# Kernel tuning notes

Measured on AMD Instinct MI355X. Metric: run time of the kernel, lower is better.

The kernel has to match this reference:

```python
import jax, jax.numpy as jnp
import numpy as np


def _rbf_kernel(X, Z, variance, lengthscale):
    # K[n, r] = variance * exp(-||x_n - z_r||^2 / (2 * lengthscale^2))
    x2 = jnp.sum(X * X, axis=-1)[:, None]          # [N, 1]
    z2 = jnp.sum(Z * Z, axis=-1)[None, :]          # [1, R]
    sq = x2 + z2 - 2.0 * (X @ Z.T)                 # [N, R]
    sq = jnp.maximum(sq, 0.0)
    return variance * jnp.exp(-0.5 * sq / (lengthscale * lengthscale))


def setup_inputs() -> dict:
    key = jax.random.key(0)
    ks = jax.random.split(key, 6)
    N, D, S, F, R = 16384, 8, 8, 1024, 2048
    X_star = jax.random.normal(ks[0], (N, D), dtype=jnp.float32)
    ref_points = jax.random.normal(ks[1], (R, D), dtype=jnp.float32)
    omega = jax.random.normal(ks[2], (S, D, F), dtype=jnp.float32)
    two_pi = 2.0 * np.pi
    phase = jax.random.uniform(ks[3], (S, F), dtype=jnp.float32) * two_pi
    feature_weights = jax.random.normal(ks[4], (S, F), dtype=jnp.float32)
    correction_weights = jax.random.normal(ks[5], (S, R), dtype=jnp.float32)
    variance = jnp.ones((), dtype=jnp.float32)
    lengthscale = jnp.ones((), dtype=jnp.float32)
    return {
        "X_star": X_star,
        "ref_points": ref_points,
        "omega": omega,
        "phase": phase,
        "feature_weights": feature_weights,
        "correction_weights": correction_weights,
        "variance": variance,
        "lengthscale": lengthscale,
    }


def reference(X_star, ref_points, omega, phase, feature_weights,
              correction_weights, variance, lengthscale):
    F = omega.shape[-1]
    # RFF prior paths: angles [S, N, F]
    angles = jnp.einsum('nd,sdf->snf', X_star, omega) / lengthscale + phase[:, None, :]
    scale = jnp.sqrt(2.0 * variance / F)
    features = scale * jnp.cos(angles)                       # [S, N, F]
    prior = jnp.sum(features * feature_weights[:, None, :], axis=-1)  # [S, N]
    # Kernel correction term
    K_cross = _rbf_kernel(X_star, ref_points, variance, lengthscale)  # [N, R]
    update = jnp.einsum('nr,sr->sn', K_cross, correction_weights)     # [S, N]
    # mean_fn is None -> zero mean
    mean = jnp.zeros(X_star.shape[0], dtype=X_star.dtype)
    return prior + update + mean[None, :]
```

## Files before the change

### kernel.cpp

```cpp
#include <hip/hip_runtime.h>
#include <math.h>

#ifndef __has_builtin
#define __has_builtin(x) 0
#endif

typedef __attribute__((ext_vector_type(8))) short bf16x8;
typedef __attribute__((ext_vector_type(4))) float f32x4;

__device__ __forceinline__ float fast_fract(float x) {
#if __has_builtin(__builtin_amdgcn_fractf)
    return __builtin_amdgcn_fractf(x);
#else
    return x - floorf(x);
#endif
}
__device__ __forceinline__ float fast_cos2pi(float x) {
#if __has_builtin(__builtin_amdgcn_cosf)
    return __builtin_amdgcn_cosf(x);
#else
    return cosf(x * 6.28318530717958647692f);
#endif
}
__device__ __forceinline__ float fast_exp2(float x) {
#if __has_builtin(__builtin_amdgcn_exp2f)
    return __builtin_amdgcn_exp2f(x);
#else
    return exp2f(x);
#endif
}
__device__ __forceinline__ unsigned short f2bf(float f) {
    unsigned u = __float_as_uint(f);
    return (unsigned short)((u + 0x7FFFu + ((u >> 16) & 1u)) >> 16);
}
__device__ __forceinline__ float bf2f(unsigned short b) {
    return __uint_as_float(((unsigned)b) << 16);
}
__device__ __forceinline__ unsigned packbf(float lo, float hi) {
    return (unsigned)f2bf(lo) | ((unsigned)f2bf(hi) << 16);
}

constexpr int kN = 16384, kD = 8, kS = 8, kF = 1024, kR = 2048;
constexpr float kInv2Pi = 0.15915494309189535f;
constexpr float kLog2e  = 1.4426950408889634f;
constexpr int kWsPrior = 512, kWsZ = 128, kWsCw = 64;
constexpr int kWsTiles = kWsPrior + kWsZ + kWsCw;
constexpr size_t kWsNeed = (size_t)kWsTiles * 64 * 16;

__global__ __launch_bounds__(256)
void prep_kernel(const float* __restrict__ omega, const float* __restrict__ phase,
                 const float* __restrict__ Z, const float* __restrict__ cw,
                 const float* __restrict__ lsp, uint4* __restrict__ ws)
{
    const int job  = blockIdx.x * 256 + threadIdx.x;
    const int lane = job & 63;
    const int tile = job >> 6;
    const int g = lane >> 4, c = lane & 15;

    const float inv_ls = 1.0f / lsp[0];
    const float m_ang  = kInv2Pi * inv_ls;
    const float L      = kLog2e * inv_ls * inv_ls;

    unsigned short h[8];
    if (tile < kWsPrior) {
        const int s = tile >> 6, ft = tile & 63, f = ft * 16 + c;
        const float* om = omega + s * (kD * kF);
        const float* ph = phase + s * kF;
        #pragma unroll
        for (int j = 0; j < 8; ++j) {
            const int k = g * 8 + j;
            unsigned short v = 0;
            if (k < 16) {
                v = f2bf(om[(k & 7) * kF + f] * m_ang);
            } else if (k < 24) {
                const float w = om[(k - 16) * kF + f] * m_ang;
                v = f2bf(w - bf2f(f2bf(w)));
            } else if (k == 24) {
                v = f2bf(ph[f] * kInv2Pi);
            } else if (k == 25) {
                const float p = ph[f] * kInv2Pi;
                v = f2bf(p - bf2f(f2bf(p)));
            }
            h[j] = v;
        }
    } else if (tile < kWsPrior + kWsZ) {
        const int rt = tile - kWsPrior;
        const int r  = rt * 16 + c;
        const float* zr = Z + r * kD;
        float zz = 0.f;
        #pragma unroll
        for (int d = 0; d < kD; ++d) zz = fmaf(zr[d], zr[d], zz);
        const float ztv = -0.5f * L * zz;
        #pragma unroll
        for (int j = 0; j < 8; ++j) {
            const int k = g * 8 + j;
            unsigned short v = 0;
            if (k < 8) {
                v = f2bf(L * zr[k]);
            } else if (k < 16) {
                v = f2bf(L * zr[k - 8]);
            } else if (k < 24) {
                const float w = L * zr[k - 16];
                v = f2bf(w - bf2f(f2bf(w)));
            } else if (k == 24) {
                v = f2bf(ztv);
            } else if (k == 25) {
                v = f2bf(ztv - bf2f(f2bf(ztv)));
            } else if (k < 28) {
                v = 0x3F80;
            }
            h[j] = v;
        }
    } else {
        const int rb = tile - kWsPrior - kWsZ;
        const int r0 = rb * 32;
        #pragma unroll
        for (int j = 0; j < 8; ++j)
            h[j] = (c < 8) ? f2bf(cw[c * kR + r0 + g * 8 + j]) : (unsigned short)0;
    }
    uint4 w;
    w.x = (unsigned)h[0] | ((unsigned)h[1] << 16);
    w.y = (unsigned)h[2] | ((unsigned)h[3] << 16);
    w.z = (unsigned)h[4] | ((unsigned)h[5] << 16);
    w.w = (unsigned)h[6] | ((unsigned)h[7] << 16);
    ws[tile * 64 + lane] = w;
}

__device__ __forceinline__ bf16x8 build_af_x(const float* __restrict__ X,
                                             int row, int g)
{
    float xv[kD];
    const float4 x0 = *reinterpret_cast<const float4*>(X + row * kD);
    const float4 x1 = *reinterpret_cast<const float4*>(X + row * kD + 4);
    xv[0]=x0.x; xv[1]=x0.y; xv[2]=x0.z; xv[3]=x0.w;
    xv[4]=x1.x; xv[5]=x1.y; xv[6]=x1.z; xv[7]=x1.w;
    bf16x8 af;
    if (g == 1) {
        #pragma unroll
        for (int j = 0; j < 8; ++j)
            af[j] = (short)f2bf(xv[j] - bf2f(f2bf(xv[j])));
    } else {
        #pragma unroll
        for (int j = 0; j < 8; ++j) af[j] = (short)f2bf(xv[j]);
    }
    return af;
}

__global__ __launch_bounds__(512, 4)
void prior_mfma3(const float* __restrict__ X, const float* __restrict__ fw,
                 const float* __restrict__ varp, const uint4* __restrict__ wsP,
                 float* __restrict__ out)
{
    __shared__ uint4 lds_b[4096];
    __shared__ float lds_fw[kF];
    const int tid  = threadIdx.x;
    const int lane = tid & 63;
    const int wave = __builtin_amdgcn_readfirstlane(tid >> 6);
    const int s  = blockIdx.y;
    const int c = lane & 15, g = lane >> 4;
    const int n0 = blockIdx.x * 256 + wave * 32;

    {
        const uint4* src = wsP + s * 4096;
        #pragma unroll
        for (int it = 0; it < 8; ++it)
            lds_b[it * 512 + tid] = src[it * 512 + tid];
        const float* fws = fw + s * kF;
        lds_fw[tid]       = fws[tid];
        lds_fw[tid + 512] = fws[tid + 512];
    }

    bf16x8 af0, af1;
    if (g == 3) {
        #pragma unroll
        for (int j = 0; j < 8; ++j) { af0[j] = 0; af1[j] = 0; }
        af0[0] = (short)0x3F80; af0[1] = (short)0x3F80;
        af1[0] = (short)0x3F80; af1[1] = (short)0x3F80;
    } else {
        af0 = build_af_x(X, n0 + c, g);
        af1 = build_af_x(X, n0 + 16 + c, g);
    }

    const float scale = sqrtf(2.0f * varp[0] / (float)kF);

    __syncthreads();

    float acc[2][4];
    #pragma unroll
    for (int t = 0; t < 2; ++t)
        #pragma unroll
        for (int r = 0; r < 4; ++r) acc[t][r] = 0.f;

    const uint4* lb = lds_b + lane;
    #pragma unroll 2
    for (int ft = 0; ft < 64; ++ft) {
        const bf16x8 bw = __builtin_bit_cast(bf16x8, lb[ft * 64]);
        const float fwv = lds_fw[ft * 16 + c];
        const f32x4 d0 = __builtin_amdgcn_mfma_f32_16x16x32_bf16(
            af0, bw, (f32x4){0.f, 0.f, 0.f, 0.f}, 0, 0, 0);
        const f32x4 d1 = __builtin_amdgcn_mfma_f32_16x16x32_bf16(
            af1, bw, (f32x4){0.f, 0.f, 0.f, 0.f}, 0, 0, 0);
        #pragma unroll
        for (int r = 0; r < 4; ++r) {
            acc[0][r] = fmaf(fwv, fast_cos2pi(fast_fract(d0[r])), acc[0][r]);
            acc[1][r] = fmaf(fwv, fast_cos2pi(fast_fract(d1[r])), acc[1][r]);
        }
    }

    #pragma unroll
    for (int m = 1; m <= 8; m <<= 1)
        #pragma unroll
        for (int t = 0; t < 2; ++t)
            #pragma unroll
            for (int r = 0; r < 4; ++r)
                acc[t][r] += __shfl_xor(acc[t][r], m);

    if (c == 0) {
        #pragma unroll
        for (int t = 0; t < 2; ++t) {
            float* o = out + s * kN + n0 + t * 16 + g * 4;
            #pragma unroll
            for (int r = 0; r < 4; ++r) o[r] = scale * acc[t][r];
        }
    }
}

__global__ __launch_bounds__(256, 2)
void update_mfma3(const float* __restrict__ X, const float* __restrict__ varp,
                  const float* __restrict__ lsp, const uint4* __restrict__ wsZ,
                  const uint4* __restrict__ wsC, float* __restrict__ out)
{
    __shared__ unsigned b2raw[4][256];
    __shared__ f32x4 red[2][2][2][16];
    const int tid  = threadIdx.x;
    const int lane = tid & 63;
    const int w    = __builtin_amdgcn_readfirstlane(tid >> 6);
    const int tl   = w >> 1, half = w & 1;
    const int tile = blockIdx.x * 2 + tl;
    const int n0   = tile * 16;
    const int c = lane & 15, g = lane >> 4;

    const float inv_ls = 1.0f / lsp[0];
    const float L = kLog2e * inv_ls * inv_ls;

    bf16x8 bf1;
    {
        float xv[kD];
        const float4 x0 = *reinterpret_cast<const float4*>(X + (n0 + c) * kD);
        const float4 x1 = *reinterpret_cast<const float4*>(X + (n0 + c) * kD + 4);
        xv[0]=x0.x; xv[1]=x0.y; xv[2]=x0.z; xv[3]=x0.w;
        xv[4]=x1.x; xv[5]=x1.y; xv[6]=x1.z; xv[7]=x1.w;
        if (g == 3) {
            float xx = 0.f;
            #pragma unroll
            for (int d = 0; d < kD; ++d) xx = fmaf(xv[d], xv[d], xx);
            const float xt = -0.5f * L * xx;
            const unsigned short th = f2bf(xt);
            const unsigned short tlw = f2bf(xt - bf2f(th));
            #pragma unroll
            for (int j = 0; j < 8; ++j) bf1[j] = 0;
            bf1[0] = (short)0x3F80; bf1[1] = (short)0x3F80;
            bf1[2] = (short)th;     bf1[3] = (short)tlw;
        } else if (g == 1) {
            #pragma unroll
            for (int j = 0; j < 8; ++j)
                bf1[j] = (short)f2bf(xv[j] - bf2f(f2bf(xv[j])));
        } else {
            #pragma unroll
            for (int j = 0; j < 8; ++j) bf1[j] = (short)f2bf(xv[j]);
        }
    }

    const int wbase = (g >> 1) * 64 + c * 4 + (g & 1) * 2;
    const int rbase = (g >> 1) * 128 + (g & 1) * 64 + c * 4;
    unsigned* bb = &b2raw[w][0];

    const uint4* zp = wsZ + lane;
    const uint4* cp = wsC + lane;
    const int rb0 = half * 32;

    f32x4 acc = {0.f, 0.f, 0.f, 0.f};
    uint4 za = zp[(rb0 * 2) * 64];
    uint4 zb = zp[(rb0 * 2 + 1) * 64];
    uint4 cf = cp[rb0 * 64];

    for (int i = 0; i < 32; ++i) {
        const int rb = rb0 + i;
        const int rbn = (i < 31) ? rb + 1 : rb;
        const uint4 zan = zp[(rbn * 2) * 64];
        const uint4 zbn = zp[(rbn * 2 + 1) * 64];
        const uint4 cfn = cp[rbn * 64];

        const f32x4 e0 = __builtin_amdgcn_mfma_f32_16x16x32_bf16(
            __builtin_bit_cast(bf16x8, za), bf1, (f32x4){0.f,0.f,0.f,0.f}, 0, 0, 0);
        const f32x4 e1 = __builtin_amdgcn_mfma_f32_16x16x32_bf16(
            __builtin_bit_cast(bf16x8, zb), bf1, (f32x4){0.f,0.f,0.f,0.f}, 0, 0, 0);

        float K0[4], K1[4];
        #pragma unroll
        for (int r = 0; r < 4; ++r) {
            K0[r] = fast_exp2(fminf(e0[r], 0.f));
            K1[r] = fast_exp2(fminf(e1[r], 0.f));
        }
        const unsigned p0 = packbf(K0[0], K0[1]);
        const unsigned p1 = packbf(K0[2], K0[3]);
        const unsigned p2 = packbf(K1[0], K1[1]);
        const unsigned p3 = packbf(K1[2], K1[3]);

        uint2 w0; w0.x = p0; w0.y = p1;
        uint2 w1; w1.x = p2; w1.y = p3;
        *reinterpret_cast<uint2*>(&bb[wbase])       = w0;
        *reinterpret_cast<uint2*>(&bb[wbase + 128]) = w1;
        const uint4 b2w = *reinterpret_cast<const uint4*>(&bb[rbase]);

        acc = __builtin_amdgcn_mfma_f32_16x16x32_bf16(
            __builtin_bit_cast(bf16x8, cf), __builtin_bit_cast(bf16x8, b2w),
            acc, 0, 0, 0);

        za = zan; zb = zbn; cf = cfn;
    }

    if (g < 2) red[tl][half][g][c] = acc;
    __syncthreads();

    {
        const int tl2 = tid >> 7, s = (tid >> 4) & 7, n = tid & 15;
        const float sum = red[tl2][0][s >> 2][n][s & 3]
                        + red[tl2][1][s >> 2][n][s & 3];
        const int idx = s * kN + (blockIdx.x * 2 + tl2) * 16 + n;
        out[idx] = fmaf(varp[0], sum, out[idx]);
    }
}

__global__ __launch_bounds__(512, 8)
void prior_fb(const float* __restrict__ X, const float* __restrict__ omega,
              const float* __restrict__ phase, const float* __restrict__ fw,
              const float* __restrict__ varp, const float* __restrict__ lsp,
              float* __restrict__ out)
{
    const int tid  = threadIdx.x;
    const int nloc = tid & 63;
    const int wave = __builtin_amdgcn_readfirstlane(tid >> 6);
    const int s    = blockIdx.y;
    const int n    = blockIdx.x * 64 + nloc;
    const float variance = varp[0];
    const float inv_ls   = 1.0f / lsp[0];
    const float scale = sqrtf(2.0f * variance / (float)kF);
    float xa[kD];
    {
        const float4 x0 = *reinterpret_cast<const float4*>(X + n * kD);
        const float4 x1 = *reinterpret_cast<const float4*>(X + n * kD + 4);
        const float m = inv_ls * kInv2Pi;
        xa[0]=x0.x*m; xa[1]=x0.y*m; xa[2]=x0.z*m; xa[3]=x0.w*m;
        xa[4]=x1.x*m; xa[5]=x1.y*m; xa[6]=x1.z*m; xa[7]=x1.w*m;
    }
    const float* om  = omega + s * (kD * kF);
    const float* ph  = phase + s * kF;
    const float* fwp = fw    + s * kF;
    const int f0 = wave * 128;
    float acc0 = 0.f, acc1 = 0.f;
    for (int fb = f0; fb < f0 + 128; fb += 8) {
        float cv[8];
        #pragma unroll
        for (int j = 0; j < 8; ++j) {
            float t = ph[fb + j] * kInv2Pi;
            #pragma unroll
            for (int d = 0; d < kD; ++d) t = fmaf(xa[d], om[d * kF + fb + j], t);
            cv[j] = fast_cos2pi(fast_fract(t));
        }
        #pragma unroll
        for (int j = 0; j < 8; j += 2) {
            acc0 = fmaf(fwp[fb + j], cv[j], acc0);
            acc1 = fmaf(fwp[fb + j + 1], cv[j + 1], acc1);
        }
    }
    __shared__ float red[8][64];
    red[wave][nloc] = acc0 + acc1;
    __syncthreads();
    if (tid < 64) {
        float t = 0.f;
        #pragma unroll
        for (int k = 0; k < 8; ++k) t += red[k][tid];
        out[s * kN + blockIdx.x * 64 + tid] = scale * t;
    }
}

__global__ __launch_bounds__(1024, 8)
void update_fb(const float* __restrict__ X, const float* __restrict__ Z,
               const float* __restrict__ cw, const float* __restrict__ varp,
               const float* __restrict__ lsp, float* __restrict__ out)
{
    const int tid  = threadIdx.x;
    const int nloc = tid & 63;
    const int wave = __builtin_amdgcn_readfirstlane(tid >> 6);
    const int n    = blockIdx.x * 64 + nloc;
    const float variance = varp[0];
    const float inv_ls   = 1.0f / lsp[0];
    const float L = kLog2e * inv_ls * inv_ls;
    __shared__ float zt_lds[kR];
    __shared__ float red[16][64][kS + 1];
    float x[kD];
    {
        const float4 x0 = *reinterpret_cast<const float4*>(X + n * kD);
        const float4 x1 = *reinterpret_cast<const float4*>(X + n * kD + 4);
        x[0]=x0.x; x[1]=x0.y; x[2]=x0.z; x[3]=x0.w;
        x[4]=x1.x; x[5]=x1.y; x[6]=x1.z; x[7]=x1.w;
    }
    for (int r = tid; r < kR; r += 1024) {
        const float4 z0 = *reinterpret_cast<const float4*>(Z + r * kD);
        const float4 z1 = *reinterpret_cast<const float4*>(Z + r * kD + 4);
        float z2 = z0.x*z0.x + z0.y*z0.y + z0.z*z0.z + z0.w*z0.w
                 + z1.x*z1.x + z1.y*z1.y + z1.z*z1.z + z1.w*z1.w;
        zt_lds[r] = -0.5f * L * z2;
    }
    __syncthreads();
    float xb[kD]; float x2 = 0.f;
    #pragma unroll
    for (int d = 0; d < kD; ++d) { xb[d] = x[d] * L; x2 = fmaf(x[d], x[d], x2); }
    const float xt = -0.5f * L * x2;
    float accU[2][kS];
    #pragma unroll
    for (int j = 0; j < kS; ++j) { accU[0][j] = 0.f; accU[1][j] = 0.f; }
    const int r0 = wave * 128;
    #pragma unroll 4
    for (int rr = 0; rr < 128; ++rr) {
        const int r = r0 + rr;
        float e = xt + zt_lds[r];
        #pragma unroll
        for (int d = 0; d < kD; ++d) e = fmaf(xb[d], Z[r * kD + d], e);
        e = fminf(e, 0.f);
        const float K = fast_exp2(e);
        #pragma unroll
        for (int j = 0; j < kS; ++j)
            accU[rr & 1][j] = fmaf(K, cw[j * kR + r], accU[rr & 1][j]);
    }
    #pragma unroll
    for (int j = 0; j < kS; ++j) red[wave][nloc][j] = accU[0][j] + accU[1][j];
    __syncthreads();
    if (tid < 512) {
        const int n2 = tid & 63;
        const int jj = tid >> 6;
        float tot = 0.f;
        #pragma unroll
        for (int k = 0; k < 16; ++k) tot += red[k][n2][jj];
        const int idx = jj * kN + blockIdx.x * 64 + n2;
        out[idx] = fmaf(variance, tot, out[idx]);
    }
}

extern "C" void kernel_launch(void* const* d_in, const int* in_sizes, int n_in,
                              void* d_out, int out_size, void* d_ws, size_t ws_size,
                              hipStream_t stream) {
    const float* X  = (const float*)d_in[0];
    const float* Z  = (const float*)d_in[1];
    const float* om = (const float*)d_in[2];
    const float* ph = (const float*)d_in[3];
    const float* fw = (const float*)d_in[4];
    const float* cw = (const float*)d_in[5];
    const float* vp = (const float*)d_in[6];
    const float* lp = (const float*)d_in[7];
    float* out = (float*)d_out;

    if (ws_size >= kWsNeed) {
        uint4* wsP = (uint4*)d_ws;
        uint4* wsZ = wsP + (size_t)kWsPrior * 64;
        uint4* wsC = wsP + (size_t)(kWsPrior + kWsZ) * 64;
        hipLaunchKernelGGL(prep_kernel, dim3(176), dim3(256), 0, stream,
                           om, ph, Z, cw, lp, wsP);
        hipLaunchKernelGGL(prior_mfma3, dim3(64, 8), dim3(512), 0, stream,
                           X, fw, vp, wsP, out);
        hipLaunchKernelGGL(update_mfma3, dim3(512), dim3(256), 0, stream,
                           X, vp, lp, wsZ, wsC, out);
    } else {
        hipLaunchKernelGGL(prior_fb, dim3(kN / 64, kS), dim3(512), 0, stream,
                           X, om, ph, fw, vp, lp, out);
        hipLaunchKernelGGL(update_fb, dim3(kN / 64), dim3(1024), 0, stream,
                           X, Z, cw, vp, lp, out);
    }
}
```

Before: 107.3 us.

## Fuse prior and update kernels into one interleaved launch with atomic accumulation

Merges the RFF prior kernel and the kernel-correction update kernel into a single launch whose blocks alternate between prior work (two of every three) and update work. The output is zeroed by extra blocks in the prep kernel, and both paths accumulate with atomicAdd, so the two phases no longer serialize across a kernel boundary and one launch is removed. The prior path now streams weights straight from global memory with a one-step register prefetch instead of staging them in LDS, which raises occupancy but adds global and atomic traffic.

```diff
diff --git a/kernel.cpp b/kernel.cpp
--- a/kernel.cpp
+++ b/kernel.cpp
@@ -50,8 +50,17 @@
 __global__ __launch_bounds__(256)
 void prep_kernel(const float* __restrict__ omega, const float* __restrict__ phase,
                  const float* __restrict__ Z, const float* __restrict__ cw,
-                 const float* __restrict__ lsp, uint4* __restrict__ ws)
+                 const float* __restrict__ lsp, uint4* __restrict__ ws,
+                 float* __restrict__ out)
 {
+    if (blockIdx.x >= 176) {
+        const int zid = (blockIdx.x - 176) * 256 + threadIdx.x;
+        float4* o4 = reinterpret_cast<float4*>(out);
+        #pragma unroll
+        for (int j = 0; j < 4; ++j)
+            o4[zid * 4 + j] = (float4){0.f, 0.f, 0.f, 0.f};
+        return;
+    }
     const int job  = blockIdx.x * 256 + threadIdx.x;
     const int lane = job & 63;
     const int tile = job >> 6;
@@ -146,189 +155,173 @@
     return af;
 }
 
-__global__ __launch_bounds__(512, 4)
-void prior_mfma3(const float* __restrict__ X, const float* __restrict__ fw,
-                 const float* __restrict__ varp, const uint4* __restrict__ wsP,
-                 float* __restrict__ out)
-{
-    __shared__ uint4 lds_b[4096];
-    __shared__ float lds_fw[kF];
-    const int tid  = threadIdx.x;
-    const int lane = tid & 63;
-    const int wave = __builtin_amdgcn_readfirstlane(tid >> 6);
-    const int s  = blockIdx.y;
-    const int c = lane & 15, g = lane >> 4;
-    const int n0 = blockIdx.x * 256 + wave * 32;
-
-    {
-        const uint4* src = wsP + s * 4096;
-        #pragma unroll
-        for (int it = 0; it < 8; ++it)
-            lds_b[it * 512 + tid] = src[it * 512 + tid];
-        const float* fws = fw + s * kF;
-        lds_fw[tid]       = fws[tid];
-        lds_fw[tid + 512] = fws[tid + 512];
-    }
-
-    bf16x8 af0, af1;
-    if (g == 3) {
-        #pragma unroll
-        for (int j = 0; j < 8; ++j) { af0[j] = 0; af1[j] = 0; }
-        af0[0] = (short)0x3F80; af0[1] = (short)0x3F80;
-        af1[0] = (short)0x3F80; af1[1] = (short)0x3F80;
-    } else {
-        af0 = build_af_x(X, n0 + c, g);
-        af1 = build_af_x(X, n0 + 16 + c, g);
-    }
-
-    const float scale = sqrtf(2.0f * varp[0] / (float)kF);
-
-    __syncthreads();
-
-    float acc[2][4];
-    #pragma unroll
-    for (int t = 0; t < 2; ++t)
-        #pragma unroll
-        for (int r = 0; r < 4; ++r) acc[t][r] = 0.f;
-
-    const uint4* lb = lds_b + lane;
-    #pragma unroll 2
-    for (int ft = 0; ft < 64; ++ft) {
-        const bf16x8 bw = __builtin_bit_cast(bf16x8, lb[ft * 64]);
-        const float fwv = lds_fw[ft * 16 + c];
-        const f32x4 d0 = __builtin_amdgcn_mfma_f32_16x16x32_bf16(
-            af0, bw, (f32x4){0.f, 0.f, 0.f, 0.f}, 0, 0, 0);
-        const f32x4 d1 = __builtin_amdgcn_mfma_f32_16x16x32_bf16(
-            af1, bw, (f32x4){0.f, 0.f, 0.f, 0.f}, 0, 0, 0);
-        #pragma unroll
-        for (int r = 0; r < 4; ++r) {
-            acc[0][r] = fmaf(fwv, fast_cos2pi(fast_fract(d0[r])), acc[0][r]);
-            acc[1][r] = fmaf(fwv, fast_cos2pi(fast_fract(d1[r])), acc[1][r]);
-        }
-    }
-
-    #pragma unroll
-    for (int m = 1; m <= 8; m <<= 1)
-        #pragma unroll
-        for (int t = 0; t < 2; ++t)
-            #pragma unroll
-            for (int r = 0; r < 4; ++r)
-                acc[t][r] += __shfl_xor(acc[t][r], m);
-
-    if (c == 0) {
-        #pragma unroll
-        for (int t = 0; t < 2; ++t) {
-            float* o = out + s * kN + n0 + t * 16 + g * 4;
-            #pragma unroll
-            for (int r = 0; r < 4; ++r) o[r] = scale * acc[t][r];
-        }
-    }
-}
-
-__global__ __launch_bounds__(256, 2)
-void update_mfma3(const float* __restrict__ X, const float* __restrict__ varp,
-                  const float* __restrict__ lsp, const uint4* __restrict__ wsZ,
-                  const uint4* __restrict__ wsC, float* __restrict__ out)
+__global__ __launch_bounds__(256, 6)
+void fused_main(const float* __restrict__ X, const float* __restrict__ fw,
+                const float* __restrict__ varp, const float* __restrict__ lsp,
+                const uint4* __restrict__ wsP, const uint4* __restrict__ wsZ,
+                const uint4* __restrict__ wsC, float* __restrict__ out)
 {
     __shared__ unsigned b2raw[4][256];
     __shared__ f32x4 red[2][2][2][16];
     const int tid  = threadIdx.x;
     const int lane = tid & 63;
     const int w    = __builtin_amdgcn_readfirstlane(tid >> 6);
-    const int tl   = w >> 1, half = w & 1;
-    const int tile = blockIdx.x * 2 + tl;
-    const int n0   = tile * 16;
     const int c = lane & 15, g = lane >> 4;
-
-    const float inv_ls = 1.0f / lsp[0];
-    const float L = kLog2e * inv_ls * inv_ls;
-
-    bf16x8 bf1;
-    {
-        float xv[kD];
-        const float4 x0 = *reinterpret_cast<const float4*>(X + (n0 + c) * kD);
-        const float4 x1 = *reinterpret_cast<const float4*>(X + (n0 + c) * kD + 4);
-        xv[0]=x0.x; xv[1]=x0.y; xv[2]=x0.z; xv[3]=x0.w;
-        xv[4]=x1.x; xv[5]=x1.y; xv[6]=x1.z; xv[7]=x1.w;
+    const int bid = blockIdx.x;
+    const int btype = bid % 3;
+
+    if (btype != 2) {
+        const int pb = (bid / 3) * 2 + btype;
+        const int s = pb & 7, ng = pb >> 3;
+        const int n0 = ng * 128 + w * 32;
+
+        bf16x8 af0, af1;
         if (g == 3) {
-            float xx = 0.f;
-            #pragma unroll
-            for (int d = 0; d < kD; ++d) xx = fmaf(xv[d], xv[d], xx);
-            const float xt = -0.5f * L * xx;
-            const unsigned short th = f2bf(xt);
-            const unsigned short tlw = f2bf(xt - bf2f(th));
-            #pragma unroll
-            for (int j = 0; j < 8; ++j) bf1[j] = 0;
-            bf1[0] = (short)0x3F80; bf1[1] = (short)0x3F80;
-            bf1[2] = (short)th;     bf1[3] = (short)tlw;
-        } else if (g == 1) {
-            #pragma unroll
-            for (int j = 0; j < 8; ++j)
-                bf1[j] = (short)f2bf(xv[j] - bf2f(f2bf(xv[j])));
+            #pragma unroll
+            for (int j = 0; j < 8; ++j) { af0[j] = 0; af1[j] = 0; }
+            af0[0] = (short)0x3F80; af0[1] = (short)0x3F80;
+            af1[0] = (short)0x3F80; af1[1] = (short)0x3F80;
         } else {
-            #pragma unroll
-            for (int j = 0; j < 8; ++j) bf1[j] = (short)f2bf(xv[j]);
-        }
-    }
-
-    const int wbase = (g >> 1) * 64 + c * 4 + (g & 1) * 2;
-    const int rbase = (g >> 1) * 128 + (g & 1) * 64 + c * 4;
-    unsigned* bb = &b2raw[w][0];
-
-    const uint4* zp = wsZ + lane;
-    const uint4* cp = wsC + lane;
-    const int rb0 = half * 32;
-
-    f32x4 acc = {0.f, 0.f, 0.f, 0.f};
-    uint4 za = zp[(rb0 * 2) * 64];
-    uint4 zb = zp[(rb0 * 2 + 1) * 64];
-    uint4 cf = cp[rb0 * 64];
-
-    for (int i = 0; i < 32; ++i) {
-        const int rb = rb0 + i;
-        const int rbn = (i < 31) ? rb + 1 : rb;
-        const uint4 zan = zp[(rbn * 2) * 64];
-        const uint4 zbn = zp[(rbn * 2 + 1) * 64];
-        const uint4 cfn = cp[rbn * 64];
-
-        const f32x4 e0 = __builtin_amdgcn_mfma_f32_16x16x32_bf16(
-            __builtin_bit_cast(bf16x8, za), bf1, (f32x4){0.f,0.f,0.f,0.f}, 0, 0, 0);
-        const f32x4 e1 = __builtin_amdgcn_mfma_f32_16x16x32_bf16(
-            __builtin_bit_cast(bf16x8, zb), bf1, (f32x4){0.f,0.f,0.f,0.f}, 0, 0, 0);
-
-        float K0[4], K1[4];
-        #pragma unroll
-        for (int r = 0; r < 4; ++r) {
-            K0[r] = fast_exp2(fminf(e0[r], 0.f));
-            K1[r] = fast_exp2(fminf(e1[r], 0.f));
-        }
-        const unsigned p0 = packbf(K0[0], K0[1]);
-        const unsigned p1 = packbf(K0[2], K0[3]);
-        const unsigned p2 = packbf(K1[0], K1[1]);
-        const unsigned p3 = packbf(K1[2], K1[3]);
-
-        uint2 w0; w0.x = p0; w0.y = p1;
-        uint2 w1; w1.x = p2; w1.y = p3;
-        *reinterpret_cast<uint2*>(&bb[wbase])       = w0;
-        *reinterpret_cast<uint2*>(&bb[wbase + 128]) = w1;
-        const uint4 b2w = *reinterpret_cast<const uint4*>(&bb[rbase]);
-
-        acc = __builtin_amdgcn_mfma_f32_16x16x32_bf16(
-            __builtin_bit_cast(bf16x8, cf), __builtin_bit_cast(bf16x8, b2w),
-            acc, 0, 0, 0);
-
-        za = zan; zb = zbn; cf = cfn;
-    }
-
-    if (g < 2) red[tl][half][g][c] = acc;
-    __syncthreads();
-
-    {
-        const int tl2 = tid >> 7, s = (tid >> 4) & 7, n = tid & 15;
-        const float sum = red[tl2][0][s >> 2][n][s & 3]
-                        + red[tl2][1][s >> 2][n][s & 3];
-        const int idx = s * kN + (blockIdx.x * 2 + tl2) * 16 + n;
-        out[idx] = fmaf(varp[0], sum, out[idx]);
+            af0 = build_af_x(X, n0 + c, g);
+            af1 = build_af_x(X, n0 + 16 + c, g);
+        }
+
+        const float scale = sqrtf(2.0f * varp[0] / (float)kF);
+        const uint4* bp  = wsP + s * 4096 + lane;
+        const float* fwp = fw + s * kF + c;
+
+        float acc[2][4];
+        #pragma unroll
+        for (int t = 0; t < 2; ++t)
+            #pragma unroll
+            for (int r = 0; r < 4; ++r) acc[t][r] = 0.f;
+
+        uint4 bw  = bp[0];
+        float fwv = fwp[0];
+        #pragma unroll 2
+        for (int ft = 0; ft < 64; ++ft) {
+            const int nx = (ft < 63) ? ft + 1 : ft;
+            const uint4 bwn  = bp[nx * 64];
+            const float fwn  = fwp[nx * 16];
+            const bf16x8 bv = __builtin_bit_cast(bf16x8, bw);
+            const f32x4 d0 = __builtin_amdgcn_mfma_f32_16x16x32_bf16(
+                af0, bv, (f32x4){0.f, 0.f, 0.f, 0.f}, 0, 0, 0);
+            const f32x4 d1 = __builtin_amdgcn_mfma_f32_16x16x32_bf16(
+                af1, bv, (f32x4){0.f, 0.f, 0.f, 0.f}, 0, 0, 0);
+            #pragma unroll
+            for (int r = 0; r < 4; ++r) {
+                acc[0][r] = fmaf(fwv, fast_cos2pi(fast_fract(d0[r])), acc[0][r]);
+                acc[1][r] = fmaf(fwv, fast_cos2pi(fast_fract(d1[r])), acc[1][r]);
+            }
+            bw = bwn; fwv = fwn;
+        }
+
+        #pragma unroll
+        for (int m = 1; m <= 8; m <<= 1)
+            #pragma unroll
+            for (int t = 0; t < 2; ++t)
+                #pragma unroll
+                for (int r = 0; r < 4; ++r)
+                    acc[t][r] += __shfl_xor(acc[t][r], m);
+
+        if (c == 0) {
+            #pragma unroll
+            for (int t = 0; t < 2; ++t) {
+                float* o = out + s * kN + n0 + t * 16 + g * 4;
+                #pragma unroll
+                for (int r = 0; r < 4; ++r) atomicAdd(o + r, scale * acc[t][r]);
+            }
+        }
+    } else {
+        const int ub   = bid / 3;
+        const int tl   = w >> 1, half = w & 1;
+        const int n0   = (ub * 2 + tl) * 16;
+
+        const float inv_ls = 1.0f / lsp[0];
+        const float L = kLog2e * inv_ls * inv_ls;
+
+        bf16x8 bf1;
+        {
+            float xv[kD];
+            const float4 x0 = *reinterpret_cast<const float4*>(X + (n0 + c) * kD);
+            const float4 x1 = *reinterpret_cast<const float4*>(X + (n0 + c) * kD + 4);
+            xv[0]=x0.x; xv[1]=x0.y; xv[2]=x0.z; xv[3]=x0.w;
+            xv[4]=x1.x; xv[5]=x1.y; xv[6]=x1.z; xv[7]=x1.w;
+            if (g == 3) {
+                float xx = 0.f;
+                #pragma unroll
+                for (int d = 0; d < kD; ++d) xx = fmaf(xv[d], xv[d], xx);
+                const float xt = -0.5f * L * xx;
+                const unsigned short th = f2bf(xt);
+                const unsigned short tlw = f2bf(xt - bf2f(th));
+                #pragma unroll
+                for (int j = 0; j < 8; ++j) bf1[j] = 0;
+                bf1[0] = (short)0x3F80; bf1[1] = (short)0x3F80;
+                bf1[2] = (short)th;     bf1[3] = (short)tlw;
+            } else if (g == 1) {
+                #pragma unroll
+                for (int j = 0; j < 8; ++j)
+                    bf1[j] = (short)f2bf(xv[j] - bf2f(f2bf(xv[j])));
+            } else {
+                #pragma unroll
+                for (int j = 0; j < 8; ++j) bf1[j] = (short)f2bf(xv[j]);
+            }
+        }
+
+        const int wbase = (g >> 1) * 64 + c * 4 + (g & 1) * 2;
+        const int rbase = (g >> 1) * 128 + (g & 1) * 64 + c * 4;
+        unsigned* bb = &b2raw[w][0];
+
+        const uint4* zp = wsZ + lane;
+        const uint4* cp = wsC + lane;
+        const int rb0 = half * 32;
+
+        f32x4 acc = {0.f, 0.f, 0.f, 0.f};
+        uint4 za = zp[(rb0 * 2) * 64];
+        uint4 zb = zp[(rb0 * 2 + 1) * 64];
+        uint4 cf = cp[rb0 * 64];
+
+        for (int i = 0; i < 32; ++i) {
+            const int rb = rb0 + i;
+            const int rbn = (i < 31) ? rb + 1 : rb;
+            const uint4 zan = zp[(rbn * 2) * 64];
+            const uint4 zbn = zp[(rbn * 2 + 1) * 64];
+            const uint4 cfn = cp[rbn * 64];
+
+            const f32x4 e0 = __builtin_amdgcn_mfma_f32_16x16x32_bf16(
+                __builtin_bit_cast(bf16x8, za), bf1, (f32x4){0.f,0.f,0.f,0.f}, 0, 0, 0);
+            const f32x4 e1 = __builtin_amdgcn_mfma_f32_16x16x32_bf16(
+                __builtin_bit_cast(bf16x8, zb), bf1, (f32x4){0.f,0.f,0.f,0.f}, 0, 0, 0);
+
+            float K0[4], K1[4];
+            #pragma unroll
+            for (int r = 0; r < 4; ++r) {
+                K0[r] = fast_exp2(fminf(e0[r], 0.f));
+                K1[r] = fast_exp2(fminf(e1[r], 0.f));
+            }
+            uint2 w0; w0.x = packbf(K0[0], K0[1]); w0.y = packbf(K0[2], K0[3]);
+            uint2 w1; w1.x = packbf(K1[0], K1[1]); w1.y = packbf(K1[2], K1[3]);
+            *reinterpret_cast<uint2*>(&bb[wbase])       = w0;
+            *reinterpret_cast<uint2*>(&bb[wbase + 128]) = w1;
+            const uint4 b2w = *reinterpret_cast<const uint4*>(&bb[rbase]);
+
+            acc = __builtin_amdgcn_mfma_f32_16x16x32_bf16(
+                __builtin_bit_cast(bf16x8, cf), __builtin_bit_cast(bf16x8, b2w),
+                acc, 0, 0, 0);
+
+            za = zan; zb = zbn; cf = cfn;
+        }
+
+        if (g < 2) red[tl][half][g][c] = acc;
+        __syncthreads();
+
+        {
+            const int tl2 = tid >> 7, s = (tid >> 4) & 7, n = tid & 15;
+            const float sum = red[tl2][0][s >> 2][n][s & 3]
+                            + red[tl2][1][s >> 2][n][s & 3];
+            const int idx = s * kN + (ub * 2 + tl2) * 16 + n;
+            atomicAdd(out + idx, varp[0] * sum);
+        }
     }
 }
 
@@ -465,12 +458,10 @@
         uint4* wsP = (uint4*)d_ws;
         uint4* wsZ = wsP + (size_t)kWsPrior * 64;
         uint4* wsC = wsP + (size_t)(kWsPrior + kWsZ) * 64;
-        hipLaunchKernelGGL(prep_kernel, dim3(176), dim3(256), 0, stream,
-                           om, ph, Z, cw, lp, wsP);
-        hipLaunchKernelGGL(prior_mfma3, dim3(64, 8), dim3(512), 0, stream,
-                           X, fw, vp, wsP, out);
-        hipLaunchKernelGGL(update_mfma3, dim3(512), dim3(256), 0, stream,
-                           X, vp, lp, wsZ, wsC, out);
+        hipLaunchKernelGGL(prep_kernel, dim3(208), dim3(256), 0, stream,
+                           om, ph, Z, cw, lp, wsP, out);
+        hipLaunchKernelGGL(fused_main, dim3(1536), dim3(256), 0, stream,
+                           X, fw, vp, lp, wsP, wsZ, wsC, out);
     } else {
         hipLaunchKernelGGL(prior_fb, dim3(kN / 64, kS), dim3(512), 0, stream,
                            X, om, ph, fw, vp, lp, out);
```

Result: faster. 101.7 us (-5.2%).
